# Kernel tuning notes

Hardware: AMD Instinct MI355X
Metric: run time of the kernel (lower is better)

## Reference

```python
import jax, jax.numpy as jnp
import numpy as np

D_MODEL = 1024
N_HEAD = 16

def setup_inputs() -> dict:
    key = jax.random.key(0)
    ks = jax.random.split(key, 11)
    B, S, D = 2, 2048, D_MODEL
    s = 1.0 / np.sqrt(D)
    inp = {
        'q': jax.random.normal(ks[0], (B, S, D), jnp.float32),
        'k': jax.random.normal(ks[1], (B, S, D), jnp.float32),
        'v': jax.random.normal(ks[2], (B, S, D), jnp.float32),
        'w_q': jax.random.normal(ks[3], (D, D), jnp.float32) * s,
        'b_q': jnp.zeros((D,), jnp.float32),
        'w_k': jax.random.normal(ks[4], (D, D), jnp.float32) * s,
        'b_k': jnp.zeros((D,), jnp.float32),
        'w_v': jax.random.normal(ks[5], (D, D), jnp.float32) * s,
        'b_v': jnp.zeros((D,), jnp.float32),
        'w_o': jax.random.normal(ks[6], (D, D), jnp.float32) * s,
        'b_o': jnp.zeros((D,), jnp.float32),
    }
    return inp

def _split_heads(x):
    B, S, D = x.shape
    return x.reshape(B, S, N_HEAD, D // N_HEAD).transpose(0, 2, 1, 3)  # [B,H,S,d]

def reference(q, k, v, w_q, b_q, w_k, b_k, w_v, b_v, w_o, b_o):
    # Linear projections (torch Linear: x @ W.T + b)
    qh = _split_heads(q @ w_q.T + b_q)
    kh = _split_heads(k @ w_k.T + b_k)
    vh = _split_heads(v @ w_v.T + b_v)
    d_k = qh.shape[-1]
    scores = jnp.einsum('bhqd,bhkd->bhqk', qh, kh) / jnp.sqrt(jnp.float32(d_k))
    attn = jax.nn.softmax(scores, axis=-1)
    out = jnp.einsum('bhqk,bhkd->bhqd', attn, vh)  # [B,H,S,d]
    B, H, S, d = out.shape
    out = out.transpose(0, 2, 1, 3).reshape(B, S, H * d)
    return out @ w_o.T + b_o
```

## Files before the change

### kernel.cpp

```cpp
#include <hip/hip_runtime.h>
#include <hip/hip_bf16.h>

typedef __hip_bfloat16 bf16;
typedef short bf16x8 __attribute__((ext_vector_type(8)));
typedef float f32x4 __attribute__((ext_vector_type(4)));

#define D_MODEL 1024
#define SEQ     2048
#define NHEAD   16
#define DHEAD   64
#define BATCH   2
#define MROWS   (BATCH*SEQ)
#define LOG2E   1.4426950408889634f

__device__ __forceinline__ void lds_dma16(const bf16* g, bf16* l) {
  __builtin_amdgcn_global_load_lds(
      (const __attribute__((address_space(1))) void*)g,
      (__attribute__((address_space(3))) void*)l, 16, 0, 0);
}

__device__ __forceinline__ uint4 pack8_f32(const float4 x0, const float4 x1) {
  union { uint4 q; bf16 h[8]; } pk;
  pk.h[0]=__float2bfloat16(x0.x); pk.h[1]=__float2bfloat16(x0.y);
  pk.h[2]=__float2bfloat16(x0.z); pk.h[3]=__float2bfloat16(x0.w);
  pk.h[4]=__float2bfloat16(x1.x); pk.h[5]=__float2bfloat16(x1.y);
  pk.h[6]=__float2bfloat16(x1.z); pk.h[7]=__float2bfloat16(x1.w);
  return pk.q;
}

__global__ __launch_bounds__(256) void convert7(
    const float* s0, const float* s1, const float* s2, const float* s3,
    const float* s4, const float* s5, const float* s6,
    bf16* d0, bf16* d1, bf16* d2, bf16* d3, bf16* d4, bf16* d5, bf16* d6)
{
  const float* S[7] = {s0,s1,s2,s3,s4,s5,s6};
  bf16*        D[7] = {d0,d1,d2,d3,d4,d5,d6};
  const int z = blockIdx.y;
  const int n8 = (z < 3) ? (MROWS*D_MODEL/8) : (D_MODEL*D_MODEL/8);
  for (int i = blockIdx.x*256 + threadIdx.x; i < n8; i += 512*256) {
    float4 a = ((const float4*)S[z])[2*i];
    float4 b = ((const float4*)S[z])[2*i+1];
    ((uint4*)D[z])[i] = pack8_f32(a, b);
  }
}

__global__ __launch_bounds__(256) void gemm3_dma(
    const bf16* A0, const bf16* A1, const bf16* A2,
    const bf16* W0, const bf16* W1, const bf16* W2,
    const float* B0, const float* B1, const float* B2,
    bf16* C0, bf16* C1, bf16* VpT)
{
  __shared__ __align__(16) bf16 As[8*128*8];
  __shared__ __align__(16) bf16 Ws[8*128*8];
  const int z = blockIdx.z;
  const bf16* A = (z == 0) ? A0 : (z == 1) ? A1 : A2;
  const bf16* W = (z == 0) ? W0 : (z == 1) ? W1 : W2;
  const float* Bv = (z == 0) ? B0 : (z == 1) ? B1 : B2;
  const bool swapped = (z < 2);
  const int K = D_MODEL, N = D_MODEL;
  const int tid  = threadIdx.x;
  const int lane = tid & 63, wave = tid >> 6;
  const int wm   = wave >> 1, wn = wave & 1;
  const int quad = lane >> 4, l16 = lane & 15;
  const int row0 = blockIdx.y * 128, col0 = blockIdx.x * 128;

  const f32x4 zero = {0.f, 0.f, 0.f, 0.f};
  f32x4 acc[4][4];
  #pragma unroll
  for (int i = 0; i < 4; ++i)
    #pragma unroll
    for (int j = 0; j < 4; ++j) acc[i][j] = zero;

  for (int k0 = 0; k0 < K; k0 += 64) {
    __syncthreads();
    #pragma unroll
    for (int t = 0; t < 4; ++t) {
      int s = t*256 + tid;
      int g = s >> 7, r = s & 127;
      lds_dma16(A + (size_t)(row0 + r)*K + k0 + g*8, &As[s*8]);
      lds_dma16(W + (size_t)(col0 + r)*K + k0 + g*8, &Ws[s*8]);
    }
    __syncthreads();
    #pragma unroll
    for (int ks = 0; ks < 2; ++ks) {
      bf16x8 af[4], wf[4];
      #pragma unroll
      for (int mt = 0; mt < 4; ++mt)
        af[mt] = *(const bf16x8*)&As[((ks*4 + quad)*128 + wm*64 + mt*16 + l16)*8];
      #pragma unroll
      for (int nt = 0; nt < 4; ++nt)
        wf[nt] = *(const bf16x8*)&Ws[((ks*4 + quad)*128 + wn*64 + nt*16 + l16)*8];
      if (swapped) {
        #pragma unroll
        for (int mt = 0; mt < 4; ++mt)
          #pragma unroll
          for (int nt = 0; nt < 4; ++nt)
            acc[mt][nt] = __builtin_amdgcn_mfma_f32_16x16x32_bf16(wf[nt], af[mt], acc[mt][nt], 0, 0, 0);
      } else {
        #pragma unroll
        for (int mt = 0; mt < 4; ++mt)
          #pragma unroll
          for (int nt = 0; nt < 4; ++nt)
            acc[mt][nt] = __builtin_amdgcn_mfma_f32_16x16x32_bf16(af[mt], wf[nt], acc[mt][nt], 0, 0, 0);
      }
    }
  }

  if (swapped) {
    bf16* C = (z == 0) ? C0 : C1;
    const float scale = (z == 0) ? 0.125f*LOG2E : 1.0f;
    #pragma unroll
    for (int mt = 0; mt < 4; ++mt) {
      int r = row0 + wm*64 + mt*16 + l16;
      #pragma unroll
      for (int nt = 0; nt < 4; ++nt) {
        int c0 = col0 + wn*64 + nt*16 + quad*4;
        float4 b4 = *(const float4*)(Bv + c0);
        union { uint2 u; bf16 h[4]; } pk;
        pk.h[0] = __float2bfloat16((acc[mt][nt][0] + b4.x) * scale);
        pk.h[1] = __float2bfloat16((acc[mt][nt][1] + b4.y) * scale);
        pk.h[2] = __float2bfloat16((acc[mt][nt][2] + b4.z) * scale);
        pk.h[3] = __float2bfloat16((acc[mt][nt][3] + b4.w) * scale);
        *(uint2*)&C[(size_t)r*N + c0] = pk.u;
      }
    }
  } else {
    const int bb = row0 >> 11;
    const int sbase = (row0 & 2047) + wm*64;
    #pragma unroll
    for (int nt = 0; nt < 4; ++nt) {
      int c = col0 + wn*64 + nt*16 + l16;
      float bv = Bv[c];
      bf16* col = VpT + (size_t)((bb << 10) + c) * SEQ;
      #pragma unroll
      for (int mt = 0; mt < 4; ++mt) {
        int s = sbase + mt*16 + quad*4;
        union { uint2 u; bf16 h[4]; } pk;
        #pragma unroll
        for (int j = 0; j < 4; ++j) pk.h[j] = __float2bfloat16(acc[mt][nt][j] + bv);
        *(uint2*)(col + s) = pk.u;
      }
    }
  }
}

__global__ __launch_bounds__(256) void gemm_out_dma(
    const bf16* __restrict__ A, const bf16* __restrict__ W,
    const float* __restrict__ Bv, float* __restrict__ C)
{
  __shared__ __align__(16) bf16 As[8*128*8];
  __shared__ __align__(16) bf16 Ws[8*64*8];
  const int K = D_MODEL, N = D_MODEL;
  const int tid  = threadIdx.x;
  const int lane = tid & 63, wave = tid >> 6;
  const int wm   = wave >> 1, wn = wave & 1;
  const int quad = lane >> 4, l16 = lane & 15;
  const int row0 = blockIdx.y * 128, col0 = blockIdx.x * 64;

  const f32x4 zero = {0.f, 0.f, 0.f, 0.f};
  f32x4 acc[4][2];
  #pragma unroll
  for (int i = 0; i < 4; ++i)
    #pragma unroll
    for (int j = 0; j < 2; ++j) acc[i][j] = zero;

  for (int k0 = 0; k0 < K; k0 += 64) {
    __syncthreads();
    #pragma unroll
    for (int t = 0; t < 4; ++t) {
      int s = t*256 + tid;
      int g = s >> 7, r = s & 127;
      lds_dma16(A + (size_t)(row0 + r)*K + k0 + g*8, &As[s*8]);
    }
    #pragma unroll
    for (int t = 0; t < 2; ++t) {
      int s = t*256 + tid;
      int g = s >> 6, r = s & 63;
      lds_dma16(W + (size_t)(col0 + r)*K + k0 + g*8, &Ws[s*8]);
    }
    __syncthreads();
    #pragma unroll
    for (int ks = 0; ks < 2; ++ks) {
      bf16x8 af[4], wf[2];
      #pragma unroll
      for (int mt = 0; mt < 4; ++mt)
        af[mt] = *(const bf16x8*)&As[((ks*4 + quad)*128 + wm*64 + mt*16 + l16)*8];
      #pragma unroll
      for (int nt = 0; nt < 2; ++nt)
        wf[nt] = *(const bf16x8*)&Ws[((ks*4 + quad)*64 + wn*32 + nt*16 + l16)*8];
      #pragma unroll
      for (int mt = 0; mt < 4; ++mt)
        #pragma unroll
        for (int nt = 0; nt < 2; ++nt)
          acc[mt][nt] = __builtin_amdgcn_mfma_f32_16x16x32_bf16(wf[nt], af[mt], acc[mt][nt], 0, 0, 0);
    }
  }

  #pragma unroll
  for (int mt = 0; mt < 4; ++mt) {
    int r = row0 + wm*64 + mt*16 + l16;
    #pragma unroll
    for (int nt = 0; nt < 2; ++nt) {
      int c0 = col0 + wn*32 + nt*16 + quad*4;
      float4 b4 = *(const float4*)(Bv + c0);
      float4 o;
      o.x = acc[mt][nt][0] + b4.x; o.y = acc[mt][nt][1] + b4.y;
      o.z = acc[mt][nt][2] + b4.z; o.w = acc[mt][nt][3] + b4.w;
      *(float4*)&C[(size_t)r*N + c0] = o;
    }
  }
}

__global__ __launch_bounds__(256) void gemm3_fused(
    const float* A0, const float* A1, const float* A2,
    const float* W0, const float* W1, const float* W2,
    const float* B0, const float* B1, const float* B2,
    bf16* C0, bf16* C1, bf16* VpT)
{
  __shared__ __align__(16) bf16 As[4*128*8];
  __shared__ __align__(16) bf16 Ws[4*128*8];
  const int z = blockIdx.z;
  const float* A = (z == 0) ? A0 : (z == 1) ? A1 : A2;
  const float* W = (z == 0) ? W0 : (z == 1) ? W1 : W2;
  const float* Bv = (z == 0) ? B0 : (z == 1) ? B1 : B2;
  const bool swapped = (z < 2);
  const int K = D_MODEL, N = D_MODEL;
  const int tid  = threadIdx.x;
  const int lane = tid & 63, wave = tid >> 6;
  const int wm   = wave >> 1, wn = wave & 1;
  const int quad = lane >> 4, l16 = lane & 15;
  const int row0 = blockIdx.y * 128, col0 = blockIdx.x * 128;

  const f32x4 zero = {0.f, 0.f, 0.f, 0.f};
  f32x4 acc[4][4];
  #pragma unroll
  for (int i = 0; i < 4; ++i)
    #pragma unroll
    for (int j = 0; j < 4; ++j) acc[i][j] = zero;

  for (int k0 = 0; k0 < K; k0 += 32) {
    __syncthreads();
    #pragma unroll
    for (int t = 0; t < 2; ++t) {
      int s = t*256 + tid;
      int g = s >> 7, r = s & 127;
      const float* Af = A + (size_t)(row0 + r)*K + k0 + g*8;
      *(uint4*)&As[s*8] = pack8_f32(((const float4*)Af)[0], ((const float4*)Af)[1]);
      const float* Wf = W + (size_t)(col0 + r)*K + k0 + g*8;
      *(uint4*)&Ws[s*8] = pack8_f32(((const float4*)Wf)[0], ((const float4*)Wf)[1]);
    }
    __syncthreads();
    bf16x8 af[4], wf[4];
    #pragma unroll
    for (int mt = 0; mt < 4; ++mt)
      af[mt] = *(const bf16x8*)&As[(quad*128 + wm*64 + mt*16 + l16)*8];
    #pragma unroll
    for (int nt = 0; nt < 4; ++nt)
      wf[nt] = *(const bf16x8*)&Ws[(quad*128 + wn*64 + nt*16 + l16)*8];
    if (swapped) {
      #pragma unroll
      for (int mt = 0; mt < 4; ++mt)
        #pragma unroll
        for (int nt = 0; nt < 4; ++nt)
          acc[mt][nt] = __builtin_amdgcn_mfma_f32_16x16x32_bf16(wf[nt], af[mt], acc[mt][nt], 0, 0, 0);
    } else {
      #pragma unroll
      for (int mt = 0; mt < 4; ++mt)
        #pragma unroll
        for (int nt = 0; nt < 4; ++nt)
          acc[mt][nt] = __builtin_amdgcn_mfma_f32_16x16x32_bf16(af[mt], wf[nt], acc[mt][nt], 0, 0, 0);
    }
  }

  if (swapped) {
    bf16* C = (z == 0) ? C0 : C1;
    const float scale = (z == 0) ? 0.125f*LOG2E : 1.0f;
    #pragma unroll
    for (int mt = 0; mt < 4; ++mt) {
      int r = row0 + wm*64 + mt*16 + l16;
      #pragma unroll
      for (int nt = 0; nt < 4; ++nt) {
        int c0 = col0 + wn*64 + nt*16 + quad*4;
        float4 b4 = *(const float4*)(Bv + c0);
        union { uint2 u; bf16 h[4]; } pk;
        pk.h[0] = __float2bfloat16((acc[mt][nt][0] + b4.x) * scale);
        pk.h[1] = __float2bfloat16((acc[mt][nt][1] + b4.y) * scale);
        pk.h[2] = __float2bfloat16((acc[mt][nt][2] + b4.z) * scale);
        pk.h[3] = __float2bfloat16((acc[mt][nt][3] + b4.w) * scale);
        *(uint2*)&C[(size_t)r*N + c0] = pk.u;
      }
    }
  } else {
    const int bb = row0 >> 11;
    const int sbase = (row0 & 2047) + wm*64;
    #pragma unroll
    for (int nt = 0; nt < 4; ++nt) {
      int c = col0 + wn*64 + nt*16 + l16;
      float bv = Bv[c];
      bf16* col = VpT + (size_t)((bb << 10) + c) * SEQ;
      #pragma unroll
      for (int mt = 0; mt < 4; ++mt) {
        int s = sbase + mt*16 + quad*4;
        union { uint2 u; bf16 h[4]; } pk;
        #pragma unroll
        for (int j = 0; j < 4; ++j) pk.h[j] = __float2bfloat16(acc[mt][nt][j] + bv);
        *(uint2*)(col + s) = pk.u;
      }
    }
  }
}

__global__ __launch_bounds__(256) void gemm_out_fused(
    const bf16* __restrict__ A, const float* __restrict__ W,
    const float* __restrict__ Bv, float* __restrict__ C)
{
  __shared__ __align__(16) bf16 As[4*128*8];
  __shared__ __align__(16) bf16 Ws[4*64*8];
  const int K = D_MODEL, N = D_MODEL;
  const int tid  = threadIdx.x;
  const int lane = tid & 63, wave = tid >> 6;
  const int wm   = wave >> 1, wn = wave & 1;
  const int quad = lane >> 4, l16 = lane & 15;
  const int row0 = blockIdx.y * 128, col0 = blockIdx.x * 64;

  const f32x4 zero = {0.f, 0.f, 0.f, 0.f};
  f32x4 acc[4][2];
  #pragma unroll
  for (int i = 0; i < 4; ++i)
    #pragma unroll
    for (int j = 0; j < 2; ++j) acc[i][j] = zero;

  for (int k0 = 0; k0 < K; k0 += 32) {
    __syncthreads();
    #pragma unroll
    for (int t = 0; t < 2; ++t) {
      int s = t*256 + tid;
      int g = s >> 7, r = s & 127;
      *(uint4*)&As[s*8] = *(const uint4*)(A + (size_t)(row0 + r)*K + k0 + g*8);
    }
    {
      int g = tid >> 6, r = tid & 63;
      const float* Wf = W + (size_t)(col0 + r)*K + k0 + g*8;
      *(uint4*)&Ws[tid*8] = pack8_f32(((const float4*)Wf)[0], ((const float4*)Wf)[1]);
    }
    __syncthreads();
    bf16x8 af[4], wf[2];
    #pragma unroll
    for (int mt = 0; mt < 4; ++mt)
      af[mt] = *(const bf16x8*)&As[(quad*128 + wm*64 + mt*16 + l16)*8];
    #pragma unroll
    for (int nt = 0; nt < 2; ++nt)
      wf[nt] = *(const bf16x8*)&Ws[(quad*64 + wn*32 + nt*16 + l16)*8];
    #pragma unroll
    for (int mt = 0; mt < 4; ++mt)
      #pragma unroll
      for (int nt = 0; nt < 2; ++nt)
        acc[mt][nt] = __builtin_amdgcn_mfma_f32_16x16x32_bf16(wf[nt], af[mt], acc[mt][nt], 0, 0, 0);
  }
  #pragma unroll
  for (int mt = 0; mt < 4; ++mt) {
    int r = row0 + wm*64 + mt*16 + l16;
    #pragma unroll
    for (int nt = 0; nt < 2; ++nt) {
      int c0 = col0 + wn*32 + nt*16 + quad*4;
      float4 b4 = *(const float4*)(Bv + c0);
      float4 o;
      o.x = acc[mt][nt][0] + b4.x; o.y = acc[mt][nt][1] + b4.y;
      o.z = acc[mt][nt][2] + b4.z; o.w = acc[mt][nt][3] + b4.w;
      *(float4*)&C[(size_t)r*N + c0] = o;
    }
  }
}

__global__ __launch_bounds__(512) void attn_fused(
    const bf16* __restrict__ Qp, const bf16* __restrict__ Kp,
    const bf16* __restrict__ VpT, bf16* __restrict__ Ao)
{
  __shared__ __align__(16) bf16 UN[128*128];
  __shared__ __align__(16) bf16 Ks[8*128*8];
  __shared__ __align__(16) bf16 Vt[64*16*8];

  const int tid  = threadIdx.x;
  const int lane = tid & 63, wave = tid >> 6;
  const int quad = lane >> 4, l16 = lane & 15;
  const int qt = blockIdx.x, h = blockIdx.y, b = blockIdx.z;
  const int q0 = qt * 128;
  const bf16* Qb = Qp + ((size_t)b*SEQ + q0)*D_MODEL + h*DHEAD;
  const bf16* Kb = Kp + (size_t)b*SEQ*D_MODEL + h*DHEAD;
  const bf16* Vg = VpT + (size_t)((b << 10) + h*DHEAD) * SEQ;

  #pragma unroll
  for (int t = 0; t < 2; ++t) {
    int s = t*512 + tid;
    int g = s >> 7, r = s & 127;
    lds_dma16(Qb + (size_t)r*D_MODEL + g*8, &UN[s*8]);
  }
  __syncthreads();

  const int wq0 = wave * 16;
  const int q   = wq0 + l16;
  bf16x8 qa[2];
  #pragma unroll
  for (int ks = 0; ks < 2; ++ks)
    qa[ks] = *(const bf16x8*)&UN[((ks*4 + quad)*128 + q)*8];
  bf16* Ps = UN;
  const int swz = (l16 & 7) << 1;

  const int vn0 = tid >> 4,        vgk0 = tid & 15;
  const int vn1 = (512+tid) >> 4,  vgk1 = (512+tid) & 15;
  const int vsw0 = (vgk0 + vn0 + (vn0 >> 3)) & 15;
  const int vsw1 = (vgk1 + vn1 + (vn1 >> 3)) & 15;
  uint4 vreg0 = *(const uint4*)(Vg + (size_t)vn0*SEQ + vgk0*8);
  uint4 vreg1 = *(const uint4*)(Vg + (size_t)vn1*SEQ + vgk1*8);

  const f32x4 zero = {0.f, 0.f, 0.f, 0.f};
  f32x4 acc_o[4];
  #pragma unroll
  for (int dt = 0; dt < 4; ++dt) acc_o[dt] = zero;
  float m_s = -1e30f, l_s = 0.f;

  for (int kt = 0; kt < SEQ/128; ++kt) {
    __syncthreads();
    #pragma unroll
    for (int t = 0; t < 2; ++t) {
      int s = t*512 + tid;
      int g = s >> 7, kk = s & 127;
      lds_dma16(Kb + (size_t)(kt*128 + kk)*D_MODEL + g*8, &Ks[s*8]);
    }
    *(uint4*)&Vt[(vn0*16 + vsw0)*8] = vreg0;
    *(uint4*)&Vt[(vn1*16 + vsw1)*8] = vreg1;
    {
      int ktn = (kt + 1 < SEQ/128) ? kt + 1 : kt;
      vreg0 = *(const uint4*)(Vg + (size_t)vn0*SEQ + ktn*128 + vgk0*8);
      vreg1 = *(const uint4*)(Vg + (size_t)vn1*SEQ + ktn*128 + vgk1*8);
    }
    __syncthreads();

    f32x4 sc[8];
    #pragma unroll
    for (int kt2 = 0; kt2 < 8; ++kt2) sc[kt2] = zero;
    #pragma unroll
    for (int ks = 0; ks < 2; ++ks) {
      bf16x8 kf[8];
      #pragma unroll
      for (int kt2 = 0; kt2 < 8; ++kt2)
        kf[kt2] = *(const bf16x8*)&Ks[((ks*4 + quad)*128 + kt2*16 + l16)*8];
      #pragma unroll
      for (int kt2 = 0; kt2 < 8; ++kt2)
        sc[kt2] = __builtin_amdgcn_mfma_f32_16x16x32_bf16(kf[kt2], qa[ks], sc[kt2], 0, 0, 0);
    }

    float vmax = -1e30f;
    #pragma unroll
    for (int kt2 = 0; kt2 < 8; ++kt2) {
      f32x4 s4 = sc[kt2];
      vmax = fmaxf(vmax, fmaxf(fmaxf(s4[0], s4[1]), fmaxf(s4[2], s4[3])));
    }
    vmax = fmaxf(vmax, __shfl_xor(vmax, 16));
    vmax = fmaxf(vmax, __shfl_xor(vmax, 32));
    float mnew  = fmaxf(m_s, vmax);
    float alpha = __builtin_amdgcn_exp2f(m_s - mnew);
    float rs = 0.f;
    #pragma unroll
    for (int kt2 = 0; kt2 < 8; ++kt2) {
      float p0 = __builtin_amdgcn_exp2f(sc[kt2][0] - mnew);
      float p1 = __builtin_amdgcn_exp2f(sc[kt2][1] - mnew);
      float p2 = __builtin_amdgcn_exp2f(sc[kt2][2] - mnew);
      float p3 = __builtin_amdgcn_exp2f(sc[kt2][3] - mnew);
      rs += (p0 + p1) + (p2 + p3);
      union { uint2 u; bf16 hh[4]; } pk;
      pk.hh[0] = __float2bfloat16(p0); pk.hh[1] = __float2bfloat16(p1);
      pk.hh[2] = __float2bfloat16(p2); pk.hh[3] = __float2bfloat16(p3);
      int phys = (kt2*4 + quad) ^ swz;
      *(uint2*)&Ps[q*128 + phys*4] = pk.u;
    }
    rs += __shfl_xor(rs, 16);
    rs += __shfl_xor(rs, 32);
    l_s = l_s*alpha + rs;
    m_s = mnew;
    #pragma unroll
    for (int dt = 0; dt < 4; ++dt) acc_o[dt] = acc_o[dt] * alpha;

    #pragma unroll
    for (int ks2 = 0; ks2 < 4; ++ks2) {
      bf16x8 vf[4], pa;
      #pragma unroll
      for (int dt = 0; dt < 4; ++dt) {
        int n = dt*16 + l16;
        int sw = (ks2*4 + quad + n + (n >> 3)) & 15;
        vf[dt] = *(const bf16x8*)&Vt[(n*16 + sw)*8];
      }
      int phys = (ks2*8 + quad*2) ^ swz;
      pa = *(const bf16x8*)&Ps[q*128 + phys*4];
      #pragma unroll
      for (int dt = 0; dt < 4; ++dt)
        acc_o[dt] = __builtin_amdgcn_mfma_f32_16x16x32_bf16(vf[dt], pa, acc_o[dt], 0, 0, 0);
    }
  }

  bf16* Ob = Ao + ((size_t)b*SEQ + q0)*D_MODEL + h*DHEAD;
  float inv = 1.f / l_s;
  #pragma unroll
  for (int dt = 0; dt < 4; ++dt) {
    union { uint2 u; bf16 hh[4]; } pk;
    #pragma unroll
    for (int j = 0; j < 4; ++j) pk.hh[j] = __float2bfloat16(acc_o[dt][j] * inv);
    *(uint2*)(Ob + (size_t)q*D_MODEL + dt*16 + quad*4) = pk.u;
  }
}

extern "C" void kernel_launch(void* const* d_in, const int* in_sizes, int n_in,
                              void* d_out, int out_size, void* d_ws, size_t ws_size,
                              hipStream_t stream) {
  const float* q   = (const float*)d_in[0];
  const float* k   = (const float*)d_in[1];
  const float* v   = (const float*)d_in[2];
  const float* w_q = (const float*)d_in[3];
  const float* b_q = (const float*)d_in[4];
  const float* w_k = (const float*)d_in[5];
  const float* b_k = (const float*)d_in[6];
  const float* w_v = (const float*)d_in[7];
  const float* b_v = (const float*)d_in[8];
  const float* w_o = (const float*)d_in[9];
  const float* b_o = (const float*)d_in[10];

  const size_t nbuf = (size_t)MROWS * D_MODEL;
  const size_t wbuf = (size_t)D_MODEL * D_MODEL;
  bf16* Kp  = (bf16*)d_out;
  bf16* VpT = Kp + nbuf;

  const size_t needA = 256 + (3*nbuf + 4*wbuf + nbuf) * 2;
  if (ws_size >= needA) {
    bf16* qc  = (bf16*)((char*)d_ws + 256);
    bf16* kc  = qc  + nbuf;
    bf16* vc  = kc  + nbuf;
    bf16* wqc = vc  + nbuf;
    bf16* wkc = wqc + wbuf;
    bf16* wvc = wkc + wbuf;
    bf16* woc = wvc + wbuf;
    bf16* Qp  = woc + wbuf;
    bf16* Ao  = Qp;

    convert7<<<dim3(512,7), 256, 0, stream>>>(q, k, v, w_q, w_k, w_v, w_o,
                                              qc, kc, vc, wqc, wkc, wvc, woc);
    gemm3_dma<<<dim3(8,32,3), 256, 0, stream>>>(qc, kc, vc, wqc, wkc, wvc,
                                                b_q, b_k, b_v, Qp, Kp, VpT);
    attn_fused<<<dim3(16,16,2), 512, 0, stream>>>(Qp, Kp, VpT, Ao);
    gemm_out_dma<<<dim3(16,32), 256, 0, stream>>>(Ao, woc, b_o, (float*)d_out);
  } else {
    bf16* Qp = (bf16*)((char*)d_ws + 256);
    bf16* Ao = Qp;
    gemm3_fused<<<dim3(8,32,3), 256, 0, stream>>>(q, k, v, w_q, w_k, w_v,
                                                  b_q, b_k, b_v, Qp, Kp, VpT);
    attn_fused<<<dim3(16,16,2), 512, 0, stream>>>(Qp, Kp, VpT, Ao);
    gemm_out_fused<<<dim3(16,32), 256, 0, stream>>>(Ao, w_o, b_o, (float*)d_out);
  }
}
```

Before: 307.0 us.

## Fuse activation fp32-to-bf16 conversion into QKV GEMM tile loads

The separate pre-conversion of the q/k/v activations to bf16 is removed. The QKV GEMM now loads fp32 activations directly, packs them to bf16 into LDS, and keeps async LDS DMA only for the pre-converted weights. This removes a full write-then-read pass over three 4M-element activation buffers and shrinks the conversion kernel to weights only. The cost is that the A-tile loads become synchronous register round-trips instead of DMA, and the unused fallback kernels are deleted.

```diff
diff --git a/kernel.cpp b/kernel.cpp
--- a/kernel.cpp
+++ b/kernel.cpp
@@ -28,24 +28,23 @@
   return pk.q;
 }
 
-__global__ __launch_bounds__(256) void convert7(
+__global__ __launch_bounds__(256) void conv_w(
     const float* s0, const float* s1, const float* s2, const float* s3,
-    const float* s4, const float* s5, const float* s6,
-    bf16* d0, bf16* d1, bf16* d2, bf16* d3, bf16* d4, bf16* d5, bf16* d6)
+    bf16* d0, bf16* d1, bf16* d2, bf16* d3)
 {
-  const float* S[7] = {s0,s1,s2,s3,s4,s5,s6};
-  bf16*        D[7] = {d0,d1,d2,d3,d4,d5,d6};
+  const float* S[4] = {s0,s1,s2,s3};
+  bf16*        D[4] = {d0,d1,d2,d3};
   const int z = blockIdx.y;
-  const int n8 = (z < 3) ? (MROWS*D_MODEL/8) : (D_MODEL*D_MODEL/8);
-  for (int i = blockIdx.x*256 + threadIdx.x; i < n8; i += 512*256) {
+  const int n8 = D_MODEL*D_MODEL/8;
+  for (int i = blockIdx.x*256 + threadIdx.x; i < n8; i += 128*256) {
     float4 a = ((const float4*)S[z])[2*i];
     float4 b = ((const float4*)S[z])[2*i+1];
     ((uint4*)D[z])[i] = pack8_f32(a, b);
   }
 }
 
-__global__ __launch_bounds__(256) void gemm3_dma(
-    const bf16* A0, const bf16* A1, const bf16* A2,
+__global__ __launch_bounds__(256) void gemm_qkv(
+    const float* A0, const float* A1, const float* A2,
     const bf16* W0, const bf16* W1, const bf16* W2,
     const float* B0, const float* B1, const float* B2,
     bf16* C0, bf16* C1, bf16* VpT)
@@ -53,8 +52,8 @@
   __shared__ __align__(16) bf16 As[8*128*8];
   __shared__ __align__(16) bf16 Ws[8*128*8];
   const int z = blockIdx.z;
-  const bf16* A = (z == 0) ? A0 : (z == 1) ? A1 : A2;
-  const bf16* W = (z == 0) ? W0 : (z == 1) ? W1 : W2;
+  const float* A = (z == 0) ? A0 : (z == 1) ? A1 : A2;
+  const bf16*  W = (z == 0) ? W0 : (z == 1) ? W1 : W2;
   const float* Bv = (z == 0) ? B0 : (z == 1) ? B1 : B2;
   const bool swapped = (z < 2);
   const int K = D_MODEL, N = D_MODEL;
@@ -77,8 +76,14 @@
     for (int t = 0; t < 4; ++t) {
       int s = t*256 + tid;
       int g = s >> 7, r = s & 127;
-      lds_dma16(A + (size_t)(row0 + r)*K + k0 + g*8, &As[s*8]);
       lds_dma16(W + (size_t)(col0 + r)*K + k0 + g*8, &Ws[s*8]);
+    }
+    #pragma unroll
+    for (int t = 0; t < 4; ++t) {
+      int s = t*256 + tid;
+      int g = s >> 7, r = s & 127;
+      const float* Af = A + (size_t)(row0 + r)*K + k0 + g*8;
+      *(uint4*)&As[s*8] = pack8_f32(((const float4*)Af)[0], ((const float4*)Af)[1]);
     }
     __syncthreads();
     #pragma unroll
@@ -211,167 +216,6 @@
   }
 }
 
-__global__ __launch_bounds__(256) void gemm3_fused(
-    const float* A0, const float* A1, const float* A2,
-    const float* W0, const float* W1, const float* W2,
-    const float* B0, const float* B1, const float* B2,
-    bf16* C0, bf16* C1, bf16* VpT)
-{
-  __shared__ __align__(16) bf16 As[4*128*8];
-  __shared__ __align__(16) bf16 Ws[4*128*8];
-  const int z = blockIdx.z;
-  const float* A = (z == 0) ? A0 : (z == 1) ? A1 : A2;
-  const float* W = (z == 0) ? W0 : (z == 1) ? W1 : W2;
-  const float* Bv = (z == 0) ? B0 : (z == 1) ? B1 : B2;
-  const bool swapped = (z < 2);
-  const int K = D_MODEL, N = D_MODEL;
-  const int tid  = threadIdx.x;
-  const int lane = tid & 63, wave = tid >> 6;
-  const int wm   = wave >> 1, wn = wave & 1;
-  const int quad = lane >> 4, l16 = lane & 15;
-  const int row0 = blockIdx.y * 128, col0 = blockIdx.x * 128;
-
-  const f32x4 zero = {0.f, 0.f, 0.f, 0.f};
-  f32x4 acc[4][4];
-  #pragma unroll
-  for (int i = 0; i < 4; ++i)
-    #pragma unroll
-    for (int j = 0; j < 4; ++j) acc[i][j] = zero;
-
-  for (int k0 = 0; k0 < K; k0 += 32) {
-    __syncthreads();
-    #pragma unroll
-    for (int t = 0; t < 2; ++t) {
-      int s = t*256 + tid;
-      int g = s >> 7, r = s & 127;
-      const float* Af = A + (size_t)(row0 + r)*K + k0 + g*8;
-      *(uint4*)&As[s*8] = pack8_f32(((const float4*)Af)[0], ((const float4*)Af)[1]);
-      const float* Wf = W + (size_t)(col0 + r)*K + k0 + g*8;
-      *(uint4*)&Ws[s*8] = pack8_f32(((const float4*)Wf)[0], ((const float4*)Wf)[1]);
-    }
-    __syncthreads();
-    bf16x8 af[4], wf[4];
-    #pragma unroll
-    for (int mt = 0; mt < 4; ++mt)
-      af[mt] = *(const bf16x8*)&As[(quad*128 + wm*64 + mt*16 + l16)*8];
-    #pragma unroll
-    for (int nt = 0; nt < 4; ++nt)
-      wf[nt] = *(const bf16x8*)&Ws[(quad*128 + wn*64 + nt*16 + l16)*8];
-    if (swapped) {
-      #pragma unroll
-      for (int mt = 0; mt < 4; ++mt)
-        #pragma unroll
-        for (int nt = 0; nt < 4; ++nt)
-          acc[mt][nt] = __builtin_amdgcn_mfma_f32_16x16x32_bf16(wf[nt], af[mt], acc[mt][nt], 0, 0, 0);
-    } else {
-      #pragma unroll
-      for (int mt = 0; mt < 4; ++mt)
-        #pragma unroll
-        for (int nt = 0; nt < 4; ++nt)
-          acc[mt][nt] = __builtin_amdgcn_mfma_f32_16x16x32_bf16(af[mt], wf[nt], acc[mt][nt], 0, 0, 0);
-    }
-  }
-
-  if (swapped) {
-    bf16* C = (z == 0) ? C0 : C1;
-    const float scale = (z == 0) ? 0.125f*LOG2E : 1.0f;
-    #pragma unroll
-    for (int mt = 0; mt < 4; ++mt) {
-      int r = row0 + wm*64 + mt*16 + l16;
-      #pragma unroll
-      for (int nt = 0; nt < 4; ++nt) {
-        int c0 = col0 + wn*64 + nt*16 + quad*4;
-        float4 b4 = *(const float4*)(Bv + c0);
-        union { uint2 u; bf16 h[4]; } pk;
-        pk.h[0] = __float2bfloat16((acc[mt][nt][0] + b4.x) * scale);
-        pk.h[1] = __float2bfloat16((acc[mt][nt][1] + b4.y) * scale);
-        pk.h[2] = __float2bfloat16((acc[mt][nt][2] + b4.z) * scale);
-        pk.h[3] = __float2bfloat16((acc[mt][nt][3] + b4.w) * scale);
-        *(uint2*)&C[(size_t)r*N + c0] = pk.u;
-      }
-    }
-  } else {
-    const int bb = row0 >> 11;
-    const int sbase = (row0 & 2047) + wm*64;
-    #pragma unroll
-    for (int nt = 0; nt < 4; ++nt) {
-      int c = col0 + wn*64 + nt*16 + l16;
-      float bv = Bv[c];
-      bf16* col = VpT + (size_t)((bb << 10) + c) * SEQ;
-      #pragma unroll
-      for (int mt = 0; mt < 4; ++mt) {
-        int s = sbase + mt*16 + quad*4;
-        union { uint2 u; bf16 h[4]; } pk;
-        #pragma unroll
-        for (int j = 0; j < 4; ++j) pk.h[j] = __float2bfloat16(acc[mt][nt][j] + bv);
-        *(uint2*)(col + s) = pk.u;
-      }
-    }
-  }
-}
-
-__global__ __launch_bounds__(256) void gemm_out_fused(
-    const bf16* __restrict__ A, const float* __restrict__ W,
-    const float* __restrict__ Bv, float* __restrict__ C)
-{
-  __shared__ __align__(16) bf16 As[4*128*8];
-  __shared__ __align__(16) bf16 Ws[4*64*8];
-  const int K = D_MODEL, N = D_MODEL;
-  const int tid  = threadIdx.x;
-  const int lane = tid & 63, wave = tid >> 6;
-  const int wm   = wave >> 1, wn = wave & 1;
-  const int quad = lane >> 4, l16 = lane & 15;
-  const int row0 = blockIdx.y * 128, col0 = blockIdx.x * 64;
-
-  const f32x4 zero = {0.f, 0.f, 0.f, 0.f};
-  f32x4 acc[4][2];
-  #pragma unroll
-  for (int i = 0; i < 4; ++i)
-    #pragma unroll
-    for (int j = 0; j < 2; ++j) acc[i][j] = zero;
-
-  for (int k0 = 0; k0 < K; k0 += 32) {
-    __syncthreads();
-    #pragma unroll
-    for (int t = 0; t < 2; ++t) {
-      int s = t*256 + tid;
-      int g = s >> 7, r = s & 127;
-      *(uint4*)&As[s*8] = *(const uint4*)(A + (size_t)(row0 + r)*K + k0 + g*8);
-    }
-    {
-      int g = tid >> 6, r = tid & 63;
-      const float* Wf = W + (size_t)(col0 + r)*K + k0 + g*8;
-      *(uint4*)&Ws[tid*8] = pack8_f32(((const float4*)Wf)[0], ((const float4*)Wf)[1]);
-    }
-    __syncthreads();
-    bf16x8 af[4], wf[2];
-    #pragma unroll
-    for (int mt = 0; mt < 4; ++mt)
-      af[mt] = *(const bf16x8*)&As[(quad*128 + wm*64 + mt*16 + l16)*8];
-    #pragma unroll
-    for (int nt = 0; nt < 2; ++nt)
-      wf[nt] = *(const bf16x8*)&Ws[(quad*64 + wn*32 + nt*16 + l16)*8];
-    #pragma unroll
-    for (int mt = 0; mt < 4; ++mt)
-      #pragma unroll
-      for (int nt = 0; nt < 2; ++nt)
-        acc[mt][nt] = __builtin_amdgcn_mfma_f32_16x16x32_bf16(wf[nt], af[mt], acc[mt][nt], 0, 0, 0);
-  }
-  #pragma unroll
-  for (int mt = 0; mt < 4; ++mt) {
-    int r = row0 + wm*64 + mt*16 + l16;
-    #pragma unroll
-    for (int nt = 0; nt < 2; ++nt) {
-      int c0 = col0 + wn*32 + nt*16 + quad*4;
-      float4 b4 = *(const float4*)(Bv + c0);
-      float4 o;
-      o.x = acc[mt][nt][0] + b4.x; o.y = acc[mt][nt][1] + b4.y;
-      o.z = acc[mt][nt][2] + b4.z; o.w = acc[mt][nt][3] + b4.w;
-      *(float4*)&C[(size_t)r*N + c0] = o;
-    }
-  }
-}
-
 __global__ __launch_bounds__(512) void attn_fused(
     const bf16* __restrict__ Qp, const bf16* __restrict__ Kp,
     const bf16* __restrict__ VpT, bf16* __restrict__ Ao)
@@ -526,33 +370,20 @@
 
   const size_t nbuf = (size_t)MROWS * D_MODEL;
   const size_t wbuf = (size_t)D_MODEL * D_MODEL;
+
+  bf16* wqc = (bf16*)d_ws;
+  bf16* wkc = wqc + wbuf;
+  bf16* wvc = wkc + wbuf;
+  bf16* woc = wvc + wbuf;
+  bf16* Qp  = woc + wbuf;
+  bf16* Ao  = Qp;
   bf16* Kp  = (bf16*)d_out;
   bf16* VpT = Kp + nbuf;
 
-  const size_t needA = 256 + (3*nbuf + 4*wbuf + nbuf) * 2;
-  if (ws_size >= needA) {
-    bf16* qc  = (bf16*)((char*)d_ws + 256);
-    bf16* kc  = qc  + nbuf;
-    bf16* vc  = kc  + nbuf;
-    bf16* wqc = vc  + nbuf;
-    bf16* wkc = wqc + wbuf;
-    bf16* wvc = wkc + wbuf;
-    bf16* woc = wvc + wbuf;
-    bf16* Qp  = woc + wbuf;
-    bf16* Ao  = Qp;
-
-    convert7<<<dim3(512,7), 256, 0, stream>>>(q, k, v, w_q, w_k, w_v, w_o,
-                                              qc, kc, vc, wqc, wkc, wvc, woc);
-    gemm3_dma<<<dim3(8,32,3), 256, 0, stream>>>(qc, kc, vc, wqc, wkc, wvc,
-                                                b_q, b_k, b_v, Qp, Kp, VpT);
-    attn_fused<<<dim3(16,16,2), 512, 0, stream>>>(Qp, Kp, VpT, Ao);
-    gemm_out_dma<<<dim3(16,32), 256, 0, stream>>>(Ao, woc, b_o, (float*)d_out);
-  } else {
-    bf16* Qp = (bf16*)((char*)d_ws + 256);
-    bf16* Ao = Qp;
-    gemm3_fused<<<dim3(8,32,3), 256, 0, stream>>>(q, k, v, w_q, w_k, w_v,
-                                                  b_q, b_k, b_v, Qp, Kp, VpT);
-    attn_fused<<<dim3(16,16,2), 512, 0, stream>>>(Qp, Kp, VpT, Ao);
-    gemm_out_fused<<<dim3(16,32), 256, 0, stream>>>(Ao, w_o, b_o, (float*)d_out);
-  }
-}
+  conv_w<<<dim3(128,4), 256, 0, stream>>>(w_q, w_k, w_v, w_o,
+                                          wqc, wkc, wvc, woc);
+  gemm_qkv<<<dim3(8,32,3), 256, 0, stream>>>(q, k, v, wqc, wkc, wvc,
+                                             b_q, b_k, b_v, Qp, Kp, VpT);
+  attn_fused<<<dim3(16,16,2), 512, 0, stream>>>(Qp, Kp, VpT, Ao);
+  gemm_out_dma<<<dim3(16,32), 256, 0, stream>>>(Ao, woc, b_o, (float*)d_out);
+}
```

Result: slower. 326.0 us (+6.2%).
